# Optimization experiments

Measured on AMD Instinct MI355X. Metric: run time of the kernel, lower is better.

Reference implementation:

```python
import jax, jax.numpy as jnp
import numpy as np

LATENT = 1024
HIDDEN = 1024
VOCAB = 32000
SEQ = 129      # y_len
STRIDE = 128   # number of decode steps = y_len - 1


def setup_inputs() -> dict:
    key = jax.random.key(0)
    ks = jax.random.split(key, 16)
    s = 0.05  # weight scale to keep gates in a sane range
    H, L, V = HIDDEN, LATENT, VOCAB
    return {
        "y": jax.random.randint(ks[0], (SEQ,), 0, V),
        "context_vector": jax.random.normal(ks[1], (2, L), jnp.float32),
        "stride": STRIDE,
        # fc_upscale: latent -> hidden
        "W_up": jax.random.normal(ks[2], (H, L), jnp.float32) * s,
        "b_up": jax.random.normal(ks[3], (H,), jnp.float32) * s,
        # LSTM layer 0 (input_size = 1), torch gate order [i, f, g, o]
        "W_ih0": jax.random.normal(ks[4], (4 * H, 1), jnp.float32) * s,
        "W_hh0": jax.random.normal(ks[5], (4 * H, H), jnp.float32) * s,
        "b_ih0": jax.random.normal(ks[6], (4 * H,), jnp.float32) * s,
        "b_hh0": jax.random.normal(ks[7], (4 * H,), jnp.float32) * s,
        # LSTM layer 1 (input_size = hidden)
        "W_ih1": jax.random.normal(ks[8], (4 * H, H), jnp.float32) * s,
        "W_hh1": jax.random.normal(ks[9], (4 * H, H), jnp.float32) * s,
        "b_ih1": jax.random.normal(ks[10], (4 * H,), jnp.float32) * s,
        "b_hh1": jax.random.normal(ks[11], (4 * H,), jnp.float32) * s,
        # fc_out: hidden -> vocab
        "W_out": jax.random.normal(ks[12], (V, H), jnp.float32) * s,
        "b_out": jax.random.normal(ks[13], (V,), jnp.float32) * s,
    }


def _lstm_cell(x, h, c, Wi, Wh, bi, bh):
    # torch nn.LSTM gate layout: [input, forget, cell(g), output]
    g = Wi @ x + bi + Wh @ h + bh          # [4H]
    i, f, gg, o = jnp.split(g, 4)
    i = jax.nn.sigmoid(i)
    f = jax.nn.sigmoid(f)
    gg = jnp.tanh(gg)
    o = jax.nn.sigmoid(o)
    c2 = f * c + i * gg
    return o * jnp.tanh(c2), c2


def reference(y, context_vector, stride, W_up, b_up,
              W_ih0, W_hh0, b_ih0, b_hh0,
              W_ih1, W_hh1, b_ih1, b_hh1,
              W_out, b_out):
    # non-bidirectional path: ctx = ctx[0] * ctx[1]; both layers share the
    # same upscaled context for h0 and c0 (torch.cat([ctx]*num_layers)).
    ctx = context_vector[0] * context_vector[1]       # [latent]
    h_init = W_up @ ctx + b_up                        # [hidden]
    tok0 = y[0].astype(jnp.float32)

    def step(carry, _):
        h0, c0, h1, c1, tok = carry
        x = tok[None]                                  # [1] LSTM input (token id as float)
        h0, c0 = _lstm_cell(x, h0, c0, W_ih0, W_hh0, b_ih0, b_hh0)
        h1, c1 = _lstm_cell(h0, h1, c1, W_ih1, W_hh1, b_ih1, b_hh1)
        preds = jax.nn.relu(W_out @ h1 + b_out)        # [vocab]
        nxt = jax.lax.stop_gradient(jnp.argmax(preds)).astype(jnp.float32)
        return (h0, c0, h1, c1, nxt), preds

    init = (h_init, h_init, h_init, h_init, tok0)
    _, outputs = jax.lax.scan(step, init, None, length=int(stride))  # [stride, vocab]
    # eval mode: log_softmax over vocab
    return jax.nn.log_softmax(outputs, axis=1)
```

## Files before the change

### kernel.cpp

```cpp
#include <hip/hip_runtime.h>

#define H 1024
#define V 32000
#define NSTEP 128
#define NLOGIT_BLK 8000

#define WS_H0   0
#define WS_C0   2048
#define WS_H1   3072
#define WS_C1   5120
#define WS_TOK  6144
#define WS_LOGZ 6145
#define WS_PMAX 8192
#define WS_PSUM 16384
#define WS_PIDX 24576

__device__ __forceinline__ float wave_dot(const float4* __restrict__ wrow4,
                                          const float4* __restrict__ v4) {
    int lane = threadIdx.x & 63;
    float acc = 0.f;
#pragma unroll
    for (int k = 0; k < 4; ++k) {
        float4 w = wrow4[lane + 64 * k];
        float4 x = v4[lane + 64 * k];
        acc += w.x * x.x + w.y * x.y + w.z * x.z + w.w * x.w;
    }
#pragma unroll
    for (int off = 32; off > 0; off >>= 1)
        acc += __shfl_down(acc, off, 64);
    return acc;
}

__device__ __forceinline__ float sigmoidf_(float x) {
    return 1.f / (1.f + expf(-x));
}

__global__ __launch_bounds__(256) void k_setup(const float* __restrict__ Wup,
                                               const float* __restrict__ bup,
                                               const float* __restrict__ cv,
                                               const int* __restrict__ y,
                                               float* __restrict__ ws) {
    int r = blockIdx.x;
    int t = threadIdx.x;
    __shared__ float red[256];
    const float* row = Wup + (size_t)r * H;
    float acc = 0.f;
    for (int j = t; j < H; j += 256) acc += row[j] * (cv[j] * cv[H + j]);
    red[t] = acc;
    __syncthreads();
    for (int s = 128; s > 0; s >>= 1) {
        if (t < s) red[t] += red[t + s];
        __syncthreads();
    }
    if (t == 0) {
        float h = red[0] + bup[r];
        ws[WS_H0 + r] = h;
        ws[WS_C0 + r] = h;
        ws[WS_H1 + r] = h;
        ws[WS_C1 + r] = h;
        if (r == 0) ws[WS_TOK] = (float)y[0];
    }
}

__global__ __launch_bounds__(256) void k_lstm0(const float* __restrict__ Whh,
                                               const float* __restrict__ Wih_col,
                                               const float* __restrict__ bih,
                                               const float* __restrict__ bhh,
                                               float* __restrict__ ws, int par) {
    __shared__ float4 shv[256];
    __shared__ float gates[4];
    int i = blockIdx.x;
    int t = threadIdx.x;
    const float* hin = ws + WS_H0 + par * H;
    shv[t] = ((const float4*)hin)[t];
    __syncthreads();
    int w = t >> 6;
    int r = i + (w << 10);
    float d = wave_dot((const float4*)(Whh + (size_t)r * H), shv);
    if ((t & 63) == 0) {
        float tok = ws[WS_TOK];
        gates[w] = d + Wih_col[r] * tok + bih[r] + bhh[r];
    }
    __syncthreads();
    if (t == 0) {
        float ig = sigmoidf_(gates[0]);
        float fg = sigmoidf_(gates[1]);
        float gg = tanhf(gates[2]);
        float og = sigmoidf_(gates[3]);
        float c = fg * ws[WS_C0 + i] + ig * gg;
        ws[WS_C0 + i] = c;
        ws[WS_H0 + (par ^ 1) * H + i] = og * tanhf(c);
    }
}

__global__ __launch_bounds__(256) void k_lstm1(const float* __restrict__ Wih,
                                               const float* __restrict__ Whh,
                                               const float* __restrict__ bih,
                                               const float* __restrict__ bhh,
                                               float* __restrict__ ws, int par) {
    __shared__ float4 shx[256];
    __shared__ float4 shh[256];
    __shared__ float gates[4];
    int i = blockIdx.x;
    int t = threadIdx.x;
    shx[t] = ((const float4*)(ws + WS_H0 + (par ^ 1) * H))[t];
    shh[t] = ((const float4*)(ws + WS_H1 + par * H))[t];
    __syncthreads();
    int w = t >> 6;
    int r = i + (w << 10);
    float d = wave_dot((const float4*)(Wih + (size_t)r * H), shx) +
              wave_dot((const float4*)(Whh + (size_t)r * H), shh);
    if ((t & 63) == 0) gates[w] = d + bih[r] + bhh[r];
    __syncthreads();
    if (t == 0) {
        float ig = sigmoidf_(gates[0]);
        float fg = sigmoidf_(gates[1]);
        float gg = tanhf(gates[2]);
        float og = sigmoidf_(gates[3]);
        float c = fg * ws[WS_C1 + i] + ig * gg;
        ws[WS_C1 + i] = c;
        ws[WS_H1 + (par ^ 1) * H + i] = og * tanhf(c);
    }
}

__global__ __launch_bounds__(256) void k_logits(const float* __restrict__ Wout,
                                                const float* __restrict__ bout,
                                                float* __restrict__ outrow,
                                                float* __restrict__ ws, int par) {
    __shared__ float4 shv[256];
    __shared__ float sval[4];
    int b = blockIdx.x;
    int t = threadIdx.x;
    shv[t] = ((const float4*)(ws + WS_H1 + (par ^ 1) * H))[t];
    __syncthreads();
    int w = t >> 6;
    int r = b * 4 + w;
    float d = wave_dot((const float4*)(Wout + (size_t)r * H), shv);
    if ((t & 63) == 0) {
        float v = d + bout[r];
        v = v > 0.f ? v : 0.f;
        outrow[r] = v;
        sval[w] = v;
    }
    __syncthreads();
    if (t == 0) {
        float m = sval[0];
        int mi = 0;
#pragma unroll
        for (int k = 1; k < 4; ++k)
            if (sval[k] > m) { m = sval[k]; mi = k; }
        float s = 0.f;
#pragma unroll
        for (int k = 0; k < 4; ++k) s += expf(sval[k] - m);
        ws[WS_PMAX + b] = m;
        ws[WS_PSUM + b] = s;
        ((int*)ws)[WS_PIDX + b] = b * 4 + mi;
    }
}

__global__ __launch_bounds__(1024) void k_reduce(float* __restrict__ ws) {
    __shared__ float sm[1024];
    __shared__ float ssum[1024];
    __shared__ int si[1024];
    int t = threadIdx.x;
    float m = -1e30f, s = 0.f;
    int idx = 0x7fffffff;
    for (int b = t; b < NLOGIT_BLK; b += 1024) {
        float bm = ws[WS_PMAX + b];
        float bs = ws[WS_PSUM + b];
        int bi = ((int*)ws)[WS_PIDX + b];
        if (bm > m) {
            s = s * expf(m - bm) + bs;
            m = bm;
            idx = bi;
        } else if (bm == m) {
            s += bs;
            if (bi < idx) idx = bi;
        } else {
            s += bs * expf(bm - m);
        }
    }
    sm[t] = m; ssum[t] = s; si[t] = idx;
    __syncthreads();
    for (int o = 512; o > 0; o >>= 1) {
        if (t < o) {
            float m2 = sm[t + o], s2 = ssum[t + o];
            int i2 = si[t + o];
            if (m2 > sm[t]) {
                ssum[t] = ssum[t] * expf(sm[t] - m2) + s2;
                sm[t] = m2;
                si[t] = i2;
            } else if (m2 == sm[t]) {
                ssum[t] += s2;
                if (i2 < si[t]) si[t] = i2;
            } else {
                ssum[t] += s2 * expf(m2 - sm[t]);
            }
        }
        __syncthreads();
    }
    if (t == 0) {
        ws[WS_LOGZ] = sm[0] + logf(ssum[0]);
        ws[WS_TOK] = (float)si[0];
    }
}

__global__ __launch_bounds__(256) void k_norm(float* __restrict__ outrow,
                                              const float* __restrict__ ws) {
    int i = blockIdx.x * 256 + threadIdx.x;
    float lz = ws[WS_LOGZ];
    if (i < V) outrow[i] -= lz;
}

extern "C" void kernel_launch(void* const* d_in, const int* in_sizes, int n_in,
                              void* d_out, int out_size, void* d_ws, size_t ws_size,
                              hipStream_t stream) {
    const int*   y    = (const int*)d_in[0];
    const float* cv   = (const float*)d_in[1];
    const float* Wup  = (const float*)d_in[3];
    const float* bup  = (const float*)d_in[4];
    const float* Wih0 = (const float*)d_in[5];
    const float* Whh0 = (const float*)d_in[6];
    const float* bih0 = (const float*)d_in[7];
    const float* bhh0 = (const float*)d_in[8];
    const float* Wih1 = (const float*)d_in[9];
    const float* Whh1 = (const float*)d_in[10];
    const float* bih1 = (const float*)d_in[11];
    const float* bhh1 = (const float*)d_in[12];
    const float* Wout = (const float*)d_in[13];
    const float* bout = (const float*)d_in[14];
    float* out = (float*)d_out;
    float* ws  = (float*)d_ws;

    k_setup<<<1024, 256, 0, stream>>>(Wup, bup, cv, y, ws);
    for (int t = 0; t < NSTEP; ++t) {
        int par = t & 1;
        k_lstm0<<<1024, 256, 0, stream>>>(Whh0, Wih0, bih0, bhh0, ws, par);
        k_lstm1<<<1024, 256, 0, stream>>>(Wih1, Whh1, bih1, bhh1, ws, par);
        k_logits<<<NLOGIT_BLK, 256, 0, stream>>>(Wout, bout, out + (size_t)t * V, ws, par);
        k_reduce<<<1, 1024, 0, stream>>>(ws);
        k_norm<<<125, 256, 0, stream>>>(out + (size_t)t * V, ws);
    }
}
```

Baseline: 5.730 ms.

## Fuse logits reduction via last-block atomics and batch normalization after loop

The logits kernel now computes 32 rows per block (8 per wave), and the last block to finish, detected by an atomic counter, performs the global max/sum/argmax reduction in-kernel. This removes the separate reduce and per-step normalize launches, so each step needs three kernels instead of five. The log-sum-exp per step is stored and a single grid-stride kernel subtracts it from all rows at the end. The cost is a serialized tail reduction in one block and fewer, larger logits blocks.

```diff
diff --git a/kernel.cpp b/kernel.cpp
--- a/kernel.cpp
+++ b/kernel.cpp
@@ -3,17 +3,20 @@
 #define H 1024
 #define V 32000
 #define NSTEP 128
-#define NLOGIT_BLK 8000
-
-#define WS_H0   0
-#define WS_C0   2048
-#define WS_H1   3072
-#define WS_C1   5120
-#define WS_TOK  6144
-#define WS_LOGZ 6145
-#define WS_PMAX 8192
-#define WS_PSUM 16384
-#define WS_PIDX 24576
+#define LBLK 1000
+#define ROWS_PER_BLK 32
+#define ROWS_PER_WAVE 8
+
+#define WS_H0    0
+#define WS_C0    2048
+#define WS_H1    3072
+#define WS_C1    5120
+#define WS_TOK   6144
+#define WS_LOGZ  6400
+#define WS_PMAX  8192
+#define WS_PSUM  10240
+#define WS_PIDX  12288
+#define WS_CNT   14336
 
 __device__ __forceinline__ float wave_dot(const float4* __restrict__ wrow4,
                                           const float4* __restrict__ v4) {
@@ -52,6 +55,7 @@
         if (t < s) red[t] += red[t + s];
         __syncthreads();
     }
+    if (r == 0 && t < NSTEP) ((int*)ws)[WS_CNT + t] = 0;
     if (t == 0) {
         float h = red[0] + bup[r];
         ws[WS_H0 + r] = h;
@@ -126,90 +130,88 @@
 __global__ __launch_bounds__(256) void k_logits(const float* __restrict__ Wout,
                                                 const float* __restrict__ bout,
                                                 float* __restrict__ outrow,
-                                                float* __restrict__ ws, int par) {
+                                                float* __restrict__ ws,
+                                                int par, int step) {
     __shared__ float4 shv[256];
-    __shared__ float sval[4];
+    __shared__ float wmax[4], wsum[4];
+    __shared__ int widx[4];
+    __shared__ int lastflag;
+    __shared__ float rm[256], rs[256];
+    __shared__ int ri[256];
     int b = blockIdx.x;
     int t = threadIdx.x;
+    int w = t >> 6, lane = t & 63;
     shv[t] = ((const float4*)(ws + WS_H1 + (par ^ 1) * H))[t];
     __syncthreads();
-    int w = t >> 6;
-    int r = b * 4 + w;
-    float d = wave_dot((const float4*)(Wout + (size_t)r * H), shv);
-    if ((t & 63) == 0) {
-        float v = d + bout[r];
-        v = v > 0.f ? v : 0.f;
-        outrow[r] = v;
-        sval[w] = v;
-    }
-    __syncthreads();
-    if (t == 0) {
-        float m = sval[0];
-        int mi = 0;
-#pragma unroll
-        for (int k = 1; k < 4; ++k)
-            if (sval[k] > m) { m = sval[k]; mi = k; }
-        float s = 0.f;
-#pragma unroll
-        for (int k = 0; k < 4; ++k) s += expf(sval[k] - m);
-        ws[WS_PMAX + b] = m;
-        ws[WS_PSUM + b] = s;
-        ((int*)ws)[WS_PIDX + b] = b * 4 + mi;
-    }
-}
-
-__global__ __launch_bounds__(1024) void k_reduce(float* __restrict__ ws) {
-    __shared__ float sm[1024];
-    __shared__ float ssum[1024];
-    __shared__ int si[1024];
-    int t = threadIdx.x;
     float m = -1e30f, s = 0.f;
-    int idx = 0x7fffffff;
-    for (int b = t; b < NLOGIT_BLK; b += 1024) {
-        float bm = ws[WS_PMAX + b];
-        float bs = ws[WS_PSUM + b];
-        int bi = ((int*)ws)[WS_PIDX + b];
-        if (bm > m) {
-            s = s * expf(m - bm) + bs;
-            m = bm;
-            idx = bi;
-        } else if (bm == m) {
-            s += bs;
-            if (bi < idx) idx = bi;
-        } else {
-            s += bs * expf(bm - m);
+    int mi = 0;
+    int rbase = b * ROWS_PER_BLK + w * ROWS_PER_WAVE;
+#pragma unroll
+    for (int k = 0; k < ROWS_PER_WAVE; ++k) {
+        int r = rbase + k;
+        float d = wave_dot((const float4*)(Wout + (size_t)r * H), shv);
+        if (lane == 0) {
+            float v = fmaxf(d + bout[r], 0.f);
+            outrow[r] = v;
+            if (v > m) { s = s * expf(m - v) + 1.f; m = v; mi = r; }
+            else       { s += expf(v - m); }
         }
     }
-    sm[t] = m; ssum[t] = s; si[t] = idx;
-    __syncthreads();
-    for (int o = 512; o > 0; o >>= 1) {
+    if (lane == 0) { wmax[w] = m; wsum[w] = s; widx[w] = mi; }
+    __syncthreads();
+    if (t == 0) {
+        float bm = wmax[0], bs = wsum[0];
+        int bi = widx[0];
+#pragma unroll
+        for (int k = 1; k < 4; ++k) {
+            float m2 = wmax[k], s2 = wsum[k];
+            int i2 = widx[k];
+            if (m2 > bm)      { bs = bs * expf(bm - m2) + s2; bm = m2; bi = i2; }
+            else if (m2 == bm){ bs += s2; if (i2 < bi) bi = i2; }
+            else              { bs += s2 * expf(m2 - bm); }
+        }
+        __hip_atomic_store(ws + WS_PMAX + b, bm, __ATOMIC_RELEASE, __HIP_MEMORY_SCOPE_AGENT);
+        __hip_atomic_store(ws + WS_PSUM + b, bs, __ATOMIC_RELEASE, __HIP_MEMORY_SCOPE_AGENT);
+        __hip_atomic_store((int*)ws + WS_PIDX + b, bi, __ATOMIC_RELEASE, __HIP_MEMORY_SCOPE_AGENT);
+        int old = __hip_atomic_fetch_add((int*)ws + WS_CNT + step, 1,
+                                         __ATOMIC_ACQ_REL, __HIP_MEMORY_SCOPE_AGENT);
+        lastflag = (old == LBLK - 1);
+    }
+    __syncthreads();
+    if (!lastflag) return;
+    float fm = -1e30f, fs = 0.f;
+    int fi = 0x7fffffff;
+    for (int i = t; i < LBLK; i += 256) {
+        float m2 = __hip_atomic_load(ws + WS_PMAX + i, __ATOMIC_ACQUIRE, __HIP_MEMORY_SCOPE_AGENT);
+        float s2 = __hip_atomic_load(ws + WS_PSUM + i, __ATOMIC_ACQUIRE, __HIP_MEMORY_SCOPE_AGENT);
+        int i2 = __hip_atomic_load((int*)ws + WS_PIDX + i, __ATOMIC_ACQUIRE, __HIP_MEMORY_SCOPE_AGENT);
+        if (m2 > fm)       { fs = fs * expf(fm - m2) + s2; fm = m2; fi = i2; }
+        else if (m2 == fm) { fs += s2; if (i2 < fi) fi = i2; }
+        else               { fs += s2 * expf(m2 - fm); }
+    }
+    rm[t] = fm; rs[t] = fs; ri[t] = fi;
+    __syncthreads();
+    for (int o = 128; o > 0; o >>= 1) {
         if (t < o) {
-            float m2 = sm[t + o], s2 = ssum[t + o];
-            int i2 = si[t + o];
-            if (m2 > sm[t]) {
-                ssum[t] = ssum[t] * expf(sm[t] - m2) + s2;
-                sm[t] = m2;
-                si[t] = i2;
-            } else if (m2 == sm[t]) {
-                ssum[t] += s2;
-                if (i2 < si[t]) si[t] = i2;
-            } else {
-                ssum[t] += s2 * expf(m2 - sm[t]);
-            }
+            float m2 = rm[t + o], s2 = rs[t + o];
+            int i2 = ri[t + o];
+            if (m2 > rm[t])       { rs[t] = rs[t] * expf(rm[t] - m2) + s2; rm[t] = m2; ri[t] = i2; }
+            else if (m2 == rm[t]) { rs[t] += s2; if (i2 < ri[t]) ri[t] = i2; }
+            else                  { rs[t] += s2 * expf(m2 - rm[t]); }
         }
         __syncthreads();
     }
     if (t == 0) {
-        ws[WS_LOGZ] = sm[0] + logf(ssum[0]);
-        ws[WS_TOK] = (float)si[0];
-    }
-}
-
-__global__ __launch_bounds__(256) void k_norm(float* __restrict__ outrow,
-                                              const float* __restrict__ ws) {
-    int i = blockIdx.x * 256 + threadIdx.x;
-    float lz = ws[WS_LOGZ];
-    if (i < V) outrow[i] -= lz;
+        ws[WS_LOGZ + step] = rm[0] + logf(rs[0]);
+        ws[WS_TOK] = (float)ri[0];
+    }
+}
+
+__global__ __launch_bounds__(256) void k_norm_all(float* __restrict__ out,
+                                                  const float* __restrict__ ws) {
+    int stride = gridDim.x * 256;
+    for (int i = blockIdx.x * 256 + threadIdx.x; i < NSTEP * V; i += stride)
+        out[i] -= ws[WS_LOGZ + i / V];
 }
 
 extern "C" void kernel_launch(void* const* d_in, const int* in_sizes, int n_in,
@@ -237,8 +239,7 @@
         int par = t & 1;
         k_lstm0<<<1024, 256, 0, stream>>>(Whh0, Wih0, bih0, bhh0, ws, par);
         k_lstm1<<<1024, 256, 0, stream>>>(Wih1, Whh1, bih1, bhh1, ws, par);
-        k_logits<<<NLOGIT_BLK, 256, 0, stream>>>(Wout, bout, out + (size_t)t * V, ws, par);
-        k_reduce<<<1, 1024, 0, stream>>>(ws);
-        k_norm<<<125, 256, 0, stream>>>(out + (size_t)t * V, ws);
-    }
-}
+        k_logits<<<LBLK, 256, 0, stream>>>(Wout, bout, out + (size_t)t * V, ws, par, t);
+    }
+    k_norm_all<<<2048, 256, 0, stream>>>(out, ws);
+}
```

Result: slower. 13.78 ms (+140.6%).

## Fuse decode loop into one persistent cooperative kernel with grid syncs

Applied to the files above, without the earlier changes.

Replaces the 640 per-step kernel launches with a single cooperative persistent kernel of 256 blocks that syncs the grid between the LSTM layers and the logits stage. The argmax/logsumexp reduction is folded into the next step, where every block redundantly reduces the 256 partials, and the log-softmax normalisation is deferred to one pass at the end. This removes launch overhead and per-step global reductions, at the cost of grid-barrier latency and fewer, fatter blocks doing the matvecs. The old multi-kernel path is kept as a fallback if the cooperative launch fails.

```diff
diff --git a/kernel.cpp b/kernel.cpp
--- a/kernel.cpp
+++ b/kernel.cpp
@@ -1,22 +1,255 @@
 #include <hip/hip_runtime.h>
+#include <hip/hip_cooperative_groups.h>
+
+namespace cg = cooperative_groups;
 
 #define H 1024
 #define V 32000
 #define NSTEP 128
-#define NLOGIT_BLK 8000
+#define NBLK 256
+#define NTHR 512
+#define RPB 125
 
 #define WS_H0   0
 #define WS_C0   2048
 #define WS_H1   3072
 #define WS_C1   5120
-#define WS_TOK  6144
-#define WS_LOGZ 6145
-#define WS_PMAX 8192
-#define WS_PSUM 16384
-#define WS_PIDX 24576
-
-__device__ __forceinline__ float wave_dot(const float4* __restrict__ wrow4,
-                                          const float4* __restrict__ v4) {
+#define WS_LOGZ 6144
+#define WS_PM   6400
+#define WS_PS   6656
+#define WS_PI   6912
+
+__device__ __forceinline__ float sigmoidf_(float x) { return 1.f / (1.f + expf(-x)); }
+
+__device__ __forceinline__ float wred(float a) {
+#pragma unroll
+    for (int o = 32; o > 0; o >>= 1) a += __shfl_down(a, o, 64);
+    return a;
+}
+
+__device__ __forceinline__ float dot_row(const float4* __restrict__ w4,
+                                         const float4* h, int lane) {
+    float a = 0.f;
+#pragma unroll
+    for (int k = 0; k < 4; ++k) {
+        float4 w = w4[lane + (k << 6)];
+        a += w.x * h[k].x + w.y * h[k].y + w.z * h[k].z + w.w * h[k].w;
+    }
+    return a;
+}
+
+__global__ __launch_bounds__(NTHR) void k_decoder(
+    const int* __restrict__ y, const float* __restrict__ cv,
+    const float* __restrict__ Wup, const float* __restrict__ bup,
+    const float* __restrict__ Wih0, const float* __restrict__ Whh0,
+    const float* __restrict__ bih0, const float* __restrict__ bhh0,
+    const float* __restrict__ Wih1, const float* __restrict__ Whh1,
+    const float* __restrict__ bih1, const float* __restrict__ bhh1,
+    const float* __restrict__ Wout, const float* __restrict__ bout,
+    float* __restrict__ out, float* __restrict__ ws)
+{
+    cg::grid_group grid = cg::this_grid();
+    const int b = blockIdx.x, t = threadIdx.x;
+    const int w = t >> 6, lane = t & 63;
+    const int gw = (b << 3) + w;
+
+    __shared__ float gl[4][4];
+    __shared__ float pm[8], psv[8];
+    __shared__ int   pix[8];
+    __shared__ float rm[NBLK], rs[NBLK];
+    __shared__ int   ri[NBLK];
+    __shared__ float s_tok;
+
+    if (gw < 1024) {
+        float4 hreg[4];
+#pragma unroll
+        for (int k = 0; k < 4; ++k) {
+            float4 a = ((const float4*)cv)[lane + (k << 6)];
+            float4 c = ((const float4*)(cv + H))[lane + (k << 6)];
+            hreg[k] = make_float4(a.x * c.x, a.y * c.y, a.z * c.z, a.w * c.w);
+        }
+        float acc = wred(dot_row((const float4*)(Wup + (size_t)gw * H), hreg, lane));
+        if (lane == 0) {
+            float h = acc + bup[gw];
+            ws[WS_H0 + gw] = h; ws[WS_C0 + gw] = h;
+            ws[WS_H1 + gw] = h; ws[WS_C1 + gw] = h;
+        }
+    }
+    grid.sync();
+
+    for (int step = 0; step < NSTEP; ++step) {
+        const int p = step & 1;
+
+        float tok;
+        if (step == 0) {
+            tok = (float)y[0];
+        } else {
+            if (t < NBLK) { rm[t] = ws[WS_PM + t]; rs[t] = ws[WS_PS + t]; ri[t] = ((const int*)ws)[WS_PI + t]; }
+            __syncthreads();
+            for (int o = NBLK >> 1; o > 0; o >>= 1) {
+                if (t < o) {
+                    float m2 = rm[t + o], s2 = rs[t + o];
+                    int i2 = ri[t + o];
+                    if (m2 > rm[t])       { rs[t] = rs[t] * expf(rm[t] - m2) + s2; rm[t] = m2; ri[t] = i2; }
+                    else if (m2 == rm[t]) { rs[t] += s2; if (i2 < ri[t]) ri[t] = i2; }
+                    else                  { rs[t] += s2 * expf(m2 - rm[t]); }
+                }
+                __syncthreads();
+            }
+            if (t == 0) {
+                s_tok = (float)ri[0];
+                if (b == 0) ws[WS_LOGZ + step - 1] = rm[0] + logf(rs[0]);
+            }
+            __syncthreads();
+            tok = s_tok;
+        }
+
+        {
+            const float4* h0o = (const float4*)(ws + WS_H0 + p * H);
+            float4 hreg[4];
+#pragma unroll
+            for (int k = 0; k < 4; ++k) hreg[k] = h0o[lane + (k << 6)];
+            const int cell = (b << 2) + (w >> 1);
+            const int r0 = cell + ((w & 1) << 11);
+            const int r1 = r0 + 1024;
+            float a0 = dot_row((const float4*)(Whh0 + (size_t)r0 * H), hreg, lane);
+            float a1 = dot_row((const float4*)(Whh0 + (size_t)r1 * H), hreg, lane);
+            a0 = wred(a0); a1 = wred(a1);
+            if (lane == 0) {
+                int gi = (w & 1) << 1;
+                gl[w >> 1][gi]     = a0 + Wih0[r0] * tok + bih0[r0] + bhh0[r0];
+                gl[w >> 1][gi + 1] = a1 + Wih0[r1] * tok + bih0[r1] + bhh0[r1];
+            }
+            __syncthreads();
+            if (t < 4) {
+                int c = (b << 2) + t;
+                float ig = sigmoidf_(gl[t][0]);
+                float fg = sigmoidf_(gl[t][1]);
+                float gg = tanhf(gl[t][2]);
+                float og = sigmoidf_(gl[t][3]);
+                float cc = fg * ws[WS_C0 + c] + ig * gg;
+                ws[WS_C0 + c] = cc;
+                ws[WS_H0 + (p ^ 1) * H + c] = og * tanhf(cc);
+            }
+        }
+        grid.sync();
+
+        {
+            const float4* h0n = (const float4*)(ws + WS_H0 + (p ^ 1) * H);
+            const float4* h1o = (const float4*)(ws + WS_H1 + p * H);
+            float4 hx[4], hh[4];
+#pragma unroll
+            for (int k = 0; k < 4; ++k) { hx[k] = h0n[lane + (k << 6)]; hh[k] = h1o[lane + (k << 6)]; }
+            const int cell = (b << 2) + (w >> 1);
+            const int r0 = cell + ((w & 1) << 11);
+            const int r1 = r0 + 1024;
+            float a0 = dot_row((const float4*)(Wih1 + (size_t)r0 * H), hx, lane)
+                     + dot_row((const float4*)(Whh1 + (size_t)r0 * H), hh, lane);
+            float a1 = dot_row((const float4*)(Wih1 + (size_t)r1 * H), hx, lane)
+                     + dot_row((const float4*)(Whh1 + (size_t)r1 * H), hh, lane);
+            a0 = wred(a0); a1 = wred(a1);
+            if (lane == 0) {
+                int gi = (w & 1) << 1;
+                gl[w >> 1][gi]     = a0 + bih1[r0] + bhh1[r0];
+                gl[w >> 1][gi + 1] = a1 + bih1[r1] + bhh1[r1];
+            }
+            __syncthreads();
+            if (t < 4) {
+                int c = (b << 2) + t;
+                float ig = sigmoidf_(gl[t][0]);
+                float fg = sigmoidf_(gl[t][1]);
+                float gg = tanhf(gl[t][2]);
+                float og = sigmoidf_(gl[t][3]);
+                float cc = fg * ws[WS_C1 + c] + ig * gg;
+                ws[WS_C1 + c] = cc;
+                ws[WS_H1 + (p ^ 1) * H + c] = og * tanhf(cc);
+            }
+        }
+        grid.sync();
+
+        {
+            const float4* h1n = (const float4*)(ws + WS_H1 + (p ^ 1) * H);
+            float4 hreg[4];
+#pragma unroll
+            for (int k = 0; k < 4; ++k) hreg[k] = h1n[lane + (k << 6)];
+            float* orow = out + (size_t)step * V;
+            const int rbase = b * RPB;
+            int rl = w << 4;
+            const int rend = (w == 7) ? RPB : (rl + 16);
+            float m = -1e30f, s = 0.f;
+            int mi = 0x7fffffff;
+            for (; rl + 1 < rend; rl += 2) {
+                int r = rbase + rl;
+                float a0 = dot_row((const float4*)(Wout + (size_t)r * H), hreg, lane);
+                float a1 = dot_row((const float4*)(Wout + (size_t)(r + 1) * H), hreg, lane);
+                a0 = wred(a0); a1 = wred(a1);
+                if (lane == 0) {
+                    float v0 = fmaxf(a0 + bout[r], 0.f);
+                    float v1 = fmaxf(a1 + bout[r + 1], 0.f);
+                    orow[r] = v0; orow[r + 1] = v1;
+                    if (v0 > m) { s = s * expf(m - v0) + 1.f; m = v0; mi = r; }     else s += expf(v0 - m);
+                    if (v1 > m) { s = s * expf(m - v1) + 1.f; m = v1; mi = r + 1; } else s += expf(v1 - m);
+                }
+            }
+            if (rl < rend) {
+                int r = rbase + rl;
+                float a0 = wred(dot_row((const float4*)(Wout + (size_t)r * H), hreg, lane));
+                if (lane == 0) {
+                    float v0 = fmaxf(a0 + bout[r], 0.f);
+                    orow[r] = v0;
+                    if (v0 > m) { s = s * expf(m - v0) + 1.f; m = v0; mi = r; } else s += expf(v0 - m);
+                }
+            }
+            if (lane == 0) { pm[w] = m; psv[w] = s; pix[w] = mi; }
+            __syncthreads();
+            if (t == 0) {
+                float bm = pm[0], bs = psv[0];
+                int bi = pix[0];
+#pragma unroll
+                for (int k = 1; k < 8; ++k) {
+                    float m2 = pm[k], s2 = psv[k];
+                    int i2 = pix[k];
+                    if (m2 > bm)       { bs = bs * expf(bm - m2) + s2; bm = m2; bi = i2; }
+                    else if (m2 == bm) { bs += s2; if (i2 < bi) bi = i2; }
+                    else               { bs += s2 * expf(m2 - bm); }
+                }
+                ws[WS_PM + b] = bm; ws[WS_PS + b] = bs; ((int*)ws)[WS_PI + b] = bi;
+            }
+        }
+        grid.sync();
+    }
+
+    if (t < NBLK) { rm[t] = ws[WS_PM + t]; rs[t] = ws[WS_PS + t]; }
+    __syncthreads();
+    for (int o = NBLK >> 1; o > 0; o >>= 1) {
+        if (t < o) {
+            float m2 = rm[t + o], s2 = rs[t + o];
+            if (m2 > rm[t])       { rs[t] = rs[t] * expf(rm[t] - m2) + s2; rm[t] = m2; }
+            else if (m2 == rm[t]) { rs[t] += s2; }
+            else                  { rs[t] += s2 * expf(m2 - rm[t]); }
+        }
+        __syncthreads();
+    }
+    if (b == 0 && t == 0) ws[WS_LOGZ + NSTEP - 1] = rm[0] + logf(rs[0]);
+    grid.sync();
+
+    for (int i = b * NTHR + t; i < NSTEP * V; i += NBLK * NTHR)
+        out[i] -= ws[WS_LOGZ + i / V];
+}
+
+#define F_NLB 8000
+#define F_H0    0
+#define F_C0    2048
+#define F_H1    3072
+#define F_C1    5120
+#define F_TOK   6144
+#define F_LOGZ  6145
+#define F_PMAX  8192
+#define F_PSUM  16384
+#define F_PIDX  24576
+
+__device__ __forceinline__ float wave_dot_s(const float4* __restrict__ wrow4,
+                                            const float4* __restrict__ v4) {
     int lane = threadIdx.x & 63;
     float acc = 0.f;
 #pragma unroll
@@ -26,159 +259,118 @@
         acc += w.x * x.x + w.y * x.y + w.z * x.z + w.w * x.w;
     }
 #pragma unroll
-    for (int off = 32; off > 0; off >>= 1)
-        acc += __shfl_down(acc, off, 64);
+    for (int off = 32; off > 0; off >>= 1) acc += __shfl_down(acc, off, 64);
     return acc;
 }
 
-__device__ __forceinline__ float sigmoidf_(float x) {
-    return 1.f / (1.f + expf(-x));
-}
-
-__global__ __launch_bounds__(256) void k_setup(const float* __restrict__ Wup,
+__global__ __launch_bounds__(256) void f_setup(const float* __restrict__ Wup,
                                                const float* __restrict__ bup,
                                                const float* __restrict__ cv,
                                                const int* __restrict__ y,
                                                float* __restrict__ ws) {
-    int r = blockIdx.x;
-    int t = threadIdx.x;
+    int r = blockIdx.x, t = threadIdx.x;
     __shared__ float red[256];
     const float* row = Wup + (size_t)r * H;
     float acc = 0.f;
     for (int j = t; j < H; j += 256) acc += row[j] * (cv[j] * cv[H + j]);
     red[t] = acc;
     __syncthreads();
-    for (int s = 128; s > 0; s >>= 1) {
-        if (t < s) red[t] += red[t + s];
-        __syncthreads();
-    }
+    for (int s = 128; s > 0; s >>= 1) { if (t < s) red[t] += red[t + s]; __syncthreads(); }
     if (t == 0) {
         float h = red[0] + bup[r];
-        ws[WS_H0 + r] = h;
-        ws[WS_C0 + r] = h;
-        ws[WS_H1 + r] = h;
-        ws[WS_C1 + r] = h;
-        if (r == 0) ws[WS_TOK] = (float)y[0];
-    }
-}
-
-__global__ __launch_bounds__(256) void k_lstm0(const float* __restrict__ Whh,
+        ws[F_H0 + r] = h; ws[F_C0 + r] = h; ws[F_H1 + r] = h; ws[F_C1 + r] = h;
+        if (r == 0) ws[F_TOK] = (float)y[0];
+    }
+}
+
+__global__ __launch_bounds__(256) void f_lstm0(const float* __restrict__ Whh,
                                                const float* __restrict__ Wih_col,
                                                const float* __restrict__ bih,
                                                const float* __restrict__ bhh,
                                                float* __restrict__ ws, int par) {
     __shared__ float4 shv[256];
     __shared__ float gates[4];
-    int i = blockIdx.x;
-    int t = threadIdx.x;
-    const float* hin = ws + WS_H0 + par * H;
-    shv[t] = ((const float4*)hin)[t];
-    __syncthreads();
-    int w = t >> 6;
-    int r = i + (w << 10);
-    float d = wave_dot((const float4*)(Whh + (size_t)r * H), shv);
-    if ((t & 63) == 0) {
-        float tok = ws[WS_TOK];
-        gates[w] = d + Wih_col[r] * tok + bih[r] + bhh[r];
-    }
+    int i = blockIdx.x, t = threadIdx.x;
+    shv[t] = ((const float4*)(ws + F_H0 + par * H))[t];
+    __syncthreads();
+    int w = t >> 6, r = i + (w << 10);
+    float d = wave_dot_s((const float4*)(Whh + (size_t)r * H), shv);
+    if ((t & 63) == 0) gates[w] = d + Wih_col[r] * ws[F_TOK] + bih[r] + bhh[r];
     __syncthreads();
     if (t == 0) {
-        float ig = sigmoidf_(gates[0]);
-        float fg = sigmoidf_(gates[1]);
-        float gg = tanhf(gates[2]);
-        float og = sigmoidf_(gates[3]);
-        float c = fg * ws[WS_C0 + i] + ig * gg;
-        ws[WS_C0 + i] = c;
-        ws[WS_H0 + (par ^ 1) * H + i] = og * tanhf(c);
-    }
-}
-
-__global__ __launch_bounds__(256) void k_lstm1(const float* __restrict__ Wih,
+        float ig = sigmoidf_(gates[0]), fg = sigmoidf_(gates[1]);
+        float gg = tanhf(gates[2]), og = sigmoidf_(gates[3]);
+        float c = fg * ws[F_C0 + i] + ig * gg;
+        ws[F_C0 + i] = c;
+        ws[F_H0 + (par ^ 1) * H + i] = og * tanhf(c);
+    }
+}
+
+__global__ __launch_bounds__(256) void f_lstm1(const float* __restrict__ Wih,
                                                const float* __restrict__ Whh,
                                                const float* __restrict__ bih,
                                                const float* __restrict__ bhh,
                                                float* __restrict__ ws, int par) {
-    __shared__ float4 shx[256];
-    __shared__ float4 shh[256];
+    __shared__ float4 shx[256], shh[256];
     __shared__ float gates[4];
-    int i = blockIdx.x;
-    int t = threadIdx.x;
-    shx[t] = ((const float4*)(ws + WS_H0 + (par ^ 1) * H))[t];
-    shh[t] = ((const float4*)(ws + WS_H1 + par * H))[t];
-    __syncthreads();
-    int w = t >> 6;
-    int r = i + (w << 10);
-    float d = wave_dot((const float4*)(Wih + (size_t)r * H), shx) +
-              wave_dot((const float4*)(Whh + (size_t)r * H), shh);
+    int i = blockIdx.x, t = threadIdx.x;
+    shx[t] = ((const float4*)(ws + F_H0 + (par ^ 1) * H))[t];
+    shh[t] = ((const float4*)(ws + F_H1 + par * H))[t];
+    __syncthreads();
+    int w = t >> 6, r = i + (w << 10);
+    float d = wave_dot_s((const float4*)(Wih + (size_t)r * H), shx) +
+              wave_dot_s((const float4*)(Whh + (size_t)r * H), shh);
     if ((t & 63) == 0) gates[w] = d + bih[r] + bhh[r];
     __syncthreads();
     if (t == 0) {
-        float ig = sigmoidf_(gates[0]);
-        float fg = sigmoidf_(gates[1]);
-        float gg = tanhf(gates[2]);
-        float og = sigmoidf_(gates[3]);
-        float c = fg * ws[WS_C1 + i] + ig * gg;
-        ws[WS_C1 + i] = c;
-        ws[WS_H1 + (par ^ 1) * H + i] = og * tanhf(c);
-    }
-}
-
-__global__ __launch_bounds__(256) void k_logits(const float* __restrict__ Wout,
+        float ig = sigmoidf_(gates[0]), fg = sigmoidf_(gates[1]);
+        float gg = tanhf(gates[2]), og = sigmoidf_(gates[3]);
+        float c = fg * ws[F_C1 + i] + ig * gg;
+        ws[F_C1 + i] = c;
+        ws[F_H1 + (par ^ 1) * H + i] = og * tanhf(c);
+    }
+}
+
+__global__ __launch_bounds__(256) void f_logits(const float* __restrict__ Wout,
                                                 const float* __restrict__ bout,
                                                 float* __restrict__ outrow,
                                                 float* __restrict__ ws, int par) {
     __shared__ float4 shv[256];
     __shared__ float sval[4];
-    int b = blockIdx.x;
-    int t = threadIdx.x;
-    shv[t] = ((const float4*)(ws + WS_H1 + (par ^ 1) * H))[t];
-    __syncthreads();
-    int w = t >> 6;
-    int r = b * 4 + w;
-    float d = wave_dot((const float4*)(Wout + (size_t)r * H), shv);
+    int b = blockIdx.x, t = threadIdx.x;
+    shv[t] = ((const float4*)(ws + F_H1 + (par ^ 1) * H))[t];
+    __syncthreads();
+    int w = t >> 6, r = b * 4 + w;
+    float d = wave_dot_s((const float4*)(Wout + (size_t)r * H), shv);
     if ((t & 63) == 0) {
-        float v = d + bout[r];
-        v = v > 0.f ? v : 0.f;
+        float v = fmaxf(d + bout[r], 0.f);
         outrow[r] = v;
         sval[w] = v;
     }
     __syncthreads();
     if (t == 0) {
-        float m = sval[0];
-        int mi = 0;
-#pragma unroll
-        for (int k = 1; k < 4; ++k)
-            if (sval[k] > m) { m = sval[k]; mi = k; }
+        float m = sval[0]; int mi = 0;
+#pragma unroll
+        for (int k = 1; k < 4; ++k) if (sval[k] > m) { m = sval[k]; mi = k; }
         float s = 0.f;
 #pragma unroll
         for (int k = 0; k < 4; ++k) s += expf(sval[k] - m);
-        ws[WS_PMAX + b] = m;
-        ws[WS_PSUM + b] = s;
-        ((int*)ws)[WS_PIDX + b] = b * 4 + mi;
-    }
-}
-
-__global__ __launch_bounds__(1024) void k_reduce(float* __restrict__ ws) {
-    __shared__ float sm[1024];
-    __shared__ float ssum[1024];
+        ws[F_PMAX + b] = m; ws[F_PSUM + b] = s; ((int*)ws)[F_PIDX + b] = b * 4 + mi;
+    }
+}
+
+__global__ __launch_bounds__(1024) void f_reduce(float* __restrict__ ws) {
+    __shared__ float sm[1024], ssum[1024];
     __shared__ int si[1024];
     int t = threadIdx.x;
     float m = -1e30f, s = 0.f;
     int idx = 0x7fffffff;
-    for (int b = t; b < NLOGIT_BLK; b += 1024) {
-        float bm = ws[WS_PMAX + b];
-        float bs = ws[WS_PSUM + b];
-        int bi = ((int*)ws)[WS_PIDX + b];
-        if (bm > m) {
-            s = s * expf(m - bm) + bs;
-            m = bm;
-            idx = bi;
-        } else if (bm == m) {
-            s += bs;
-            if (bi < idx) idx = bi;
-        } else {
-            s += bs * expf(bm - m);
-        }
+    for (int b = t; b < F_NLB; b += 1024) {
+        float bm = ws[F_PMAX + b], bs = ws[F_PSUM + b];
+        int bi = ((int*)ws)[F_PIDX + b];
+        if (bm > m)      { s = s * expf(m - bm) + bs; m = bm; idx = bi; }
+        else if (bm == m){ s += bs; if (bi < idx) idx = bi; }
+        else             { s += bs * expf(bm - m); }
     }
     sm[t] = m; ssum[t] = s; si[t] = idx;
     __syncthreads();
@@ -186,30 +378,19 @@
         if (t < o) {
             float m2 = sm[t + o], s2 = ssum[t + o];
             int i2 = si[t + o];
-            if (m2 > sm[t]) {
-                ssum[t] = ssum[t] * expf(sm[t] - m2) + s2;
-                sm[t] = m2;
-                si[t] = i2;
-            } else if (m2 == sm[t]) {
-                ssum[t] += s2;
-                if (i2 < si[t]) si[t] = i2;
-            } else {
-                ssum[t] += s2 * expf(m2 - sm[t]);
-            }
+            if (m2 > sm[t])       { ssum[t] = ssum[t] * expf(sm[t] - m2) + s2; sm[t] = m2; si[t] = i2; }
+            else if (m2 == sm[t]) { ssum[t] += s2; if (i2 < si[t]) si[t] = i2; }
+            else                  { ssum[t] += s2 * expf(m2 - sm[t]); }
         }
         __syncthreads();
     }
-    if (t == 0) {
-        ws[WS_LOGZ] = sm[0] + logf(ssum[0]);
-        ws[WS_TOK] = (float)si[0];
-    }
-}
-
-__global__ __launch_bounds__(256) void k_norm(float* __restrict__ outrow,
+    if (t == 0) { ws[F_LOGZ] = sm[0] + logf(ssum[0]); ws[F_TOK] = (float)si[0]; }
+}
+
+__global__ __launch_bounds__(256) void f_norm(float* __restrict__ outrow,
                                               const float* __restrict__ ws) {
     int i = blockIdx.x * 256 + threadIdx.x;
-    float lz = ws[WS_LOGZ];
-    if (i < V) outrow[i] -= lz;
+    if (i < V) outrow[i] -= ws[F_LOGZ];
 }
 
 extern "C" void kernel_launch(void* const* d_in, const int* in_sizes, int n_in,
@@ -232,13 +413,23 @@
     float* out = (float*)d_out;
     float* ws  = (float*)d_ws;
 
-    k_setup<<<1024, 256, 0, stream>>>(Wup, bup, cv, y, ws);
-    for (int t = 0; t < NSTEP; ++t) {
-        int par = t & 1;
-        k_lstm0<<<1024, 256, 0, stream>>>(Whh0, Wih0, bih0, bhh0, ws, par);
-        k_lstm1<<<1024, 256, 0, stream>>>(Wih1, Whh1, bih1, bhh1, ws, par);
-        k_logits<<<NLOGIT_BLK, 256, 0, stream>>>(Wout, bout, out + (size_t)t * V, ws, par);
-        k_reduce<<<1, 1024, 0, stream>>>(ws);
-        k_norm<<<125, 256, 0, stream>>>(out + (size_t)t * V, ws);
-    }
-}
+    void* args[] = {
+        (void*)&y, (void*)&cv, (void*)&Wup, (void*)&bup,
+        (void*)&Wih0, (void*)&Whh0, (void*)&bih0, (void*)&bhh0,
+        (void*)&Wih1, (void*)&Whh1, (void*)&bih1, (void*)&bhh1,
+        (void*)&Wout, (void*)&bout, (void*)&out, (void*)&ws
+    };
+    hipError_t err = hipLaunchCooperativeKernel((void*)k_decoder, dim3(NBLK), dim3(NTHR),
+                                                args, 0, stream);
+    if (err != hipSuccess) {
+        f_setup<<<1024, 256, 0, stream>>>(Wup, bup, cv, y, ws);
+        for (int t = 0; t < NSTEP; ++t) {
+            int par = t & 1;
+            f_lstm0<<<1024, 256, 0, stream>>>(Whh0, Wih0, bih0, bhh0, ws, par);
+            f_lstm1<<<1024, 256, 0, stream>>>(Wih1, Whh1, bih1, bhh1, ws, par);
+            f_logits<<<F_NLB, 256, 0, stream>>>(Wout, bout, out + (size_t)t * V, ws, par);
+            f_reduce<<<1, 1024, 0, stream>>>(ws);
+            f_norm<<<125, 256, 0, stream>>>(out + (size_t)t * V, ws);
+        }
+    }
+}
```

New measurement: 13.34 ms. 133% more time.

## Fuse LSTM layers per step, precompute next layer-0 gates, defer log-softmax

Applied to the files above, without the earlier changes.

Merges the two LSTM layer kernels and the argmax reduction into a single per-step kernel. Each block redundantly reduces the previous step's argmax, applies the layer-0 cell elementwise from precomputed gate pre-activations, computes its slice of layer-1 gates, and computes the next step's layer-0 recurrent matvec. The logits kernel now handles 16 rows per block and emits only a partial max and index. Softmax normalisation moves to one batched kernel after all steps. Together these cut per-step launches from five to two, in exchange for redundant argmax and layer-0 elementwise work in every block.

```diff
diff --git a/kernel.cpp b/kernel.cpp
--- a/kernel.cpp
+++ b/kernel.cpp
@@ -3,123 +3,169 @@
 #define H 1024
 #define V 32000
 #define NSTEP 128
-#define NLOGIT_BLK 8000
-
-#define WS_H0   0
-#define WS_C0   2048
-#define WS_H1   3072
-#define WS_C1   5120
-#define WS_TOK  6144
-#define WS_LOGZ 6145
-#define WS_PMAX 8192
-#define WS_PSUM 16384
-#define WS_PIDX 24576
-
-__device__ __forceinline__ float wave_dot(const float4* __restrict__ wrow4,
-                                          const float4* __restrict__ v4) {
-    int lane = threadIdx.x & 63;
-    float acc = 0.f;
+#define LBLK 2000
+#define LROWS 16
+#define NBLK_L 256
+#define NTHR_L 512
+
+#define WS_G0    0
+#define WS_HINIT 8192
+#define WS_C0    9216
+#define WS_H1    11264
+#define WS_C1    13312
+#define WS_PMAX  14336
+#define WS_PIDX  16384
+
+__device__ __forceinline__ float sigmoidf_(float x) { return 1.f / (1.f + expf(-x)); }
+
+__device__ __forceinline__ float wred(float a) {
+#pragma unroll
+    for (int o = 32; o > 0; o >>= 1) a += __shfl_down(a, o, 64);
+    return a;
+}
+
+__device__ __forceinline__ float dot_row(const float4* __restrict__ w4,
+                                         const float4* h, int lane) {
+    float a = 0.f;
 #pragma unroll
     for (int k = 0; k < 4; ++k) {
-        float4 w = wrow4[lane + 64 * k];
-        float4 x = v4[lane + 64 * k];
-        acc += w.x * x.x + w.y * x.y + w.z * x.z + w.w * x.w;
-    }
-#pragma unroll
-    for (int off = 32; off > 0; off >>= 1)
-        acc += __shfl_down(acc, off, 64);
-    return acc;
-}
-
-__device__ __forceinline__ float sigmoidf_(float x) {
-    return 1.f / (1.f + expf(-x));
+        float4 w = w4[lane + (k << 6)];
+        a += w.x * h[k].x + w.y * h[k].y + w.z * h[k].z + w.w * h[k].w;
+    }
+    return a;
 }
 
 __global__ __launch_bounds__(256) void k_setup(const float* __restrict__ Wup,
                                                const float* __restrict__ bup,
                                                const float* __restrict__ cv,
-                                               const int* __restrict__ y,
                                                float* __restrict__ ws) {
-    int r = blockIdx.x;
-    int t = threadIdx.x;
+    int r = blockIdx.x, t = threadIdx.x;
     __shared__ float red[256];
     const float* row = Wup + (size_t)r * H;
     float acc = 0.f;
     for (int j = t; j < H; j += 256) acc += row[j] * (cv[j] * cv[H + j]);
     red[t] = acc;
     __syncthreads();
-    for (int s = 128; s > 0; s >>= 1) {
-        if (t < s) red[t] += red[t + s];
-        __syncthreads();
-    }
+    for (int s = 128; s > 0; s >>= 1) { if (t < s) red[t] += red[t + s]; __syncthreads(); }
     if (t == 0) {
         float h = red[0] + bup[r];
-        ws[WS_H0 + r] = h;
+        ws[WS_HINIT + r] = h;
         ws[WS_C0 + r] = h;
         ws[WS_H1 + r] = h;
         ws[WS_C1 + r] = h;
-        if (r == 0) ws[WS_TOK] = (float)y[0];
-    }
-}
-
-__global__ __launch_bounds__(256) void k_lstm0(const float* __restrict__ Whh,
-                                               const float* __restrict__ Wih_col,
-                                               const float* __restrict__ bih,
-                                               const float* __restrict__ bhh,
-                                               float* __restrict__ ws, int par) {
-    __shared__ float4 shv[256];
-    __shared__ float gates[4];
-    int i = blockIdx.x;
-    int t = threadIdx.x;
-    const float* hin = ws + WS_H0 + par * H;
-    shv[t] = ((const float4*)hin)[t];
-    __syncthreads();
-    int w = t >> 6;
-    int r = i + (w << 10);
-    float d = wave_dot((const float4*)(Whh + (size_t)r * H), shv);
-    if ((t & 63) == 0) {
-        float tok = ws[WS_TOK];
-        gates[w] = d + Wih_col[r] * tok + bih[r] + bhh[r];
-    }
-    __syncthreads();
-    if (t == 0) {
-        float ig = sigmoidf_(gates[0]);
-        float fg = sigmoidf_(gates[1]);
-        float gg = tanhf(gates[2]);
-        float og = sigmoidf_(gates[3]);
-        float c = fg * ws[WS_C0 + i] + ig * gg;
-        ws[WS_C0 + i] = c;
-        ws[WS_H0 + (par ^ 1) * H + i] = og * tanhf(c);
-    }
-}
-
-__global__ __launch_bounds__(256) void k_lstm1(const float* __restrict__ Wih,
-                                               const float* __restrict__ Whh,
-                                               const float* __restrict__ bih,
-                                               const float* __restrict__ bhh,
-                                               float* __restrict__ ws, int par) {
-    __shared__ float4 shx[256];
-    __shared__ float4 shh[256];
-    __shared__ float gates[4];
-    int i = blockIdx.x;
-    int t = threadIdx.x;
-    shx[t] = ((const float4*)(ws + WS_H0 + (par ^ 1) * H))[t];
-    shh[t] = ((const float4*)(ws + WS_H1 + par * H))[t];
-    __syncthreads();
-    int w = t >> 6;
-    int r = i + (w << 10);
-    float d = wave_dot((const float4*)(Wih + (size_t)r * H), shx) +
-              wave_dot((const float4*)(Whh + (size_t)r * H), shh);
-    if ((t & 63) == 0) gates[w] = d + bih[r] + bhh[r];
-    __syncthreads();
-    if (t == 0) {
-        float ig = sigmoidf_(gates[0]);
-        float fg = sigmoidf_(gates[1]);
-        float gg = tanhf(gates[2]);
-        float og = sigmoidf_(gates[3]);
-        float c = fg * ws[WS_C1 + i] + ig * gg;
-        ws[WS_C1 + i] = c;
-        ws[WS_H1 + (par ^ 1) * H + i] = og * tanhf(c);
+    }
+}
+
+__global__ __launch_bounds__(256) void k_g0(const float* __restrict__ Whh0,
+                                            const float* __restrict__ bih0,
+                                            const float* __restrict__ bhh0,
+                                            float* __restrict__ ws) {
+    int b = blockIdx.x, t = threadIdx.x;
+    int w = t >> 6, lane = t & 63;
+    float4 hreg[4];
+#pragma unroll
+    for (int k = 0; k < 4; ++k) hreg[k] = ((const float4*)(ws + WS_HINIT))[lane + (k << 6)];
+    int r = (b << 2) + w;
+    float a = wred(dot_row((const float4*)(Whh0 + (size_t)r * H), hreg, lane));
+    if (lane == 0) ws[WS_G0 + r] = a + bih0[r] + bhh0[r];
+}
+
+__global__ __launch_bounds__(NTHR_L) void k_L(
+    const int* __restrict__ y,
+    const float* __restrict__ Wih0col,
+    const float* __restrict__ Whh0,
+    const float* __restrict__ bih0, const float* __restrict__ bhh0,
+    const float* __restrict__ Wih1, const float* __restrict__ Whh1,
+    const float* __restrict__ bih1, const float* __restrict__ bhh1,
+    float* __restrict__ ws, int step)
+{
+    const int b = blockIdx.x, t = threadIdx.x;
+    const int w = t >> 6, lane = t & 63;
+    const int p = step & 1;
+    __shared__ float h0s[H];
+    __shared__ float rm[NTHR_L];
+    __shared__ int   ri[NTHR_L];
+    __shared__ float gl[4][4];
+
+    float tok;
+    if (step == 0) {
+        tok = (float)y[0];
+    } else {
+        float m = -1e30f;
+        int idx = 0x7fffffff;
+        for (int i = t; i < LBLK; i += NTHR_L) {
+            float m2 = ws[WS_PMAX + i];
+            int i2 = ((const int*)ws)[WS_PIDX + i];
+            if (m2 > m || (m2 == m && i2 < idx)) {
+                if (m2 > m) { m = m2; idx = i2; }
+                else if (i2 < idx) idx = i2;
+            }
+        }
+        rm[t] = m; ri[t] = idx;
+        __syncthreads();
+        for (int o = NTHR_L >> 1; o > 0; o >>= 1) {
+            if (t < o) {
+                float m2 = rm[t + o]; int i2 = ri[t + o];
+                if (m2 > rm[t]) { rm[t] = m2; ri[t] = i2; }
+                else if (m2 == rm[t] && i2 < ri[t]) ri[t] = i2;
+            }
+            __syncthreads();
+        }
+        tok = (float)ri[0];
+    }
+
+    for (int c = t; c < H; c += NTHR_L) {
+        float gi = ws[WS_G0 + p * 4096 + c]        + Wih0col[c]        * tok;
+        float gf = ws[WS_G0 + p * 4096 + 1024 + c] + Wih0col[1024 + c] * tok;
+        float gg = ws[WS_G0 + p * 4096 + 2048 + c] + Wih0col[2048 + c] * tok;
+        float go = ws[WS_G0 + p * 4096 + 3072 + c] + Wih0col[3072 + c] * tok;
+        float cc = sigmoidf_(gf) * ws[WS_C0 + p * H + c] + sigmoidf_(gi) * tanhf(gg);
+        ws[WS_C0 + (p ^ 1) * H + c] = cc;
+        h0s[c] = sigmoidf_(go) * tanhf(cc);
+    }
+    __syncthreads();
+
+    float4 hx[4], hh[4];
+#pragma unroll
+    for (int k = 0; k < 4; ++k) {
+        hx[k] = ((const float4*)h0s)[lane + (k << 6)];
+        hh[k] = ((const float4*)(ws + WS_H1 + p * H))[lane + (k << 6)];
+    }
+    {
+        const int cell = (b << 2) + (w >> 1);
+        const int r0 = cell + ((w & 1) << 11);
+        const int r1 = r0 + 1024;
+        float a0 = dot_row((const float4*)(Wih1 + (size_t)r0 * H), hx, lane)
+                 + dot_row((const float4*)(Whh1 + (size_t)r0 * H), hh, lane);
+        float a1 = dot_row((const float4*)(Wih1 + (size_t)r1 * H), hx, lane)
+                 + dot_row((const float4*)(Whh1 + (size_t)r1 * H), hh, lane);
+        a0 = wred(a0); a1 = wred(a1);
+        if (lane == 0) {
+            int gi = (w & 1) << 1;
+            gl[w >> 1][gi]     = a0 + bih1[r0] + bhh1[r0];
+            gl[w >> 1][gi + 1] = a1 + bih1[r1] + bhh1[r1];
+        }
+    }
+    {
+        const int g0r = (b << 4) + (w << 1);
+        float b0 = dot_row((const float4*)(Whh0 + (size_t)g0r * H), hx, lane);
+        float b1 = dot_row((const float4*)(Whh0 + (size_t)(g0r + 1) * H), hx, lane);
+        b0 = wred(b0); b1 = wred(b1);
+        if (lane == 0) {
+            ws[WS_G0 + (p ^ 1) * 4096 + g0r]     = b0 + bih0[g0r] + bhh0[g0r];
+            ws[WS_G0 + (p ^ 1) * 4096 + g0r + 1] = b1 + bih0[g0r + 1] + bhh0[g0r + 1];
+        }
+    }
+    __syncthreads();
+    if (t < 4) {
+        int cell = (b << 2) + t;
+        float ig = sigmoidf_(gl[t][0]);
+        float fg = sigmoidf_(gl[t][1]);
+        float gg = tanhf(gl[t][2]);
+        float og = sigmoidf_(gl[t][3]);
+        float cc = fg * ws[WS_C1 + cell] + ig * gg;
+        ws[WS_C1 + cell] = cc;
+        ws[WS_H1 + (p ^ 1) * H + cell] = og * tanhf(cc);
     }
 }
 
@@ -127,89 +173,67 @@
                                                 const float* __restrict__ bout,
                                                 float* __restrict__ outrow,
                                                 float* __restrict__ ws, int par) {
-    __shared__ float4 shv[256];
-    __shared__ float sval[4];
-    int b = blockIdx.x;
-    int t = threadIdx.x;
-    shv[t] = ((const float4*)(ws + WS_H1 + (par ^ 1) * H))[t];
-    __syncthreads();
-    int w = t >> 6;
-    int r = b * 4 + w;
-    float d = wave_dot((const float4*)(Wout + (size_t)r * H), shv);
-    if ((t & 63) == 0) {
-        float v = d + bout[r];
-        v = v > 0.f ? v : 0.f;
-        outrow[r] = v;
-        sval[w] = v;
-    }
+    __shared__ float pm[4];
+    __shared__ int   pix[4];
+    int b = blockIdx.x, t = threadIdx.x;
+    int w = t >> 6, lane = t & 63;
+    float4 hreg[4];
+#pragma unroll
+    for (int k = 0; k < 4; ++k)
+        hreg[k] = ((const float4*)(ws + WS_H1 + par * H))[lane + (k << 6)];
+    float m = -1e30f;
+    int mi = 0x7fffffff;
+    const int rbase = b * LROWS + (w << 2);
+#pragma unroll
+    for (int rr = 0; rr < 4; rr += 2) {
+        int r = rbase + rr;
+        float a0 = dot_row((const float4*)(Wout + (size_t)r * H), hreg, lane);
+        float a1 = dot_row((const float4*)(Wout + (size_t)(r + 1) * H), hreg, lane);
+        a0 = wred(a0); a1 = wred(a1);
+        if (lane == 0) {
+            float v0 = fmaxf(a0 + bout[r], 0.f);
+            float v1 = fmaxf(a1 + bout[r + 1], 0.f);
+            outrow[r] = v0; outrow[r + 1] = v1;
+            if (v0 > m) { m = v0; mi = r; }
+            if (v1 > m) { m = v1; mi = r + 1; }
+        }
+    }
+    if (lane == 0) { pm[w] = m; pix[w] = mi; }
     __syncthreads();
     if (t == 0) {
-        float m = sval[0];
-        int mi = 0;
-#pragma unroll
-        for (int k = 1; k < 4; ++k)
-            if (sval[k] > m) { m = sval[k]; mi = k; }
-        float s = 0.f;
-#pragma unroll
-        for (int k = 0; k < 4; ++k) s += expf(sval[k] - m);
-        ws[WS_PMAX + b] = m;
-        ws[WS_PSUM + b] = s;
-        ((int*)ws)[WS_PIDX + b] = b * 4 + mi;
-    }
-}
-
-__global__ __launch_bounds__(1024) void k_reduce(float* __restrict__ ws) {
-    __shared__ float sm[1024];
-    __shared__ float ssum[1024];
-    __shared__ int si[1024];
-    int t = threadIdx.x;
-    float m = -1e30f, s = 0.f;
-    int idx = 0x7fffffff;
-    for (int b = t; b < NLOGIT_BLK; b += 1024) {
-        float bm = ws[WS_PMAX + b];
-        float bs = ws[WS_PSUM + b];
-        int bi = ((int*)ws)[WS_PIDX + b];
-        if (bm > m) {
-            s = s * expf(m - bm) + bs;
-            m = bm;
-            idx = bi;
-        } else if (bm == m) {
-            s += bs;
-            if (bi < idx) idx = bi;
-        } else {
-            s += bs * expf(bm - m);
-        }
-    }
-    sm[t] = m; ssum[t] = s; si[t] = idx;
+        float bm = pm[0]; int bi = pix[0];
+#pragma unroll
+        for (int k = 1; k < 4; ++k) {
+            if (pm[k] > bm) { bm = pm[k]; bi = pix[k]; }
+            else if (pm[k] == bm && pix[k] < bi) bi = pix[k];
+        }
+        ws[WS_PMAX + b] = bm;
+        ((int*)ws)[WS_PIDX + b] = bi;
+    }
+}
+
+__global__ __launch_bounds__(1024) void k_final(float* __restrict__ out) {
+    __shared__ float rm[1024], rs[1024];
+    int s = blockIdx.x, t = threadIdx.x;
+    float* row = out + (size_t)s * V;
+    float m = -1e30f, sum = 0.f;
+    for (int i = t; i < V; i += 1024) {
+        float v = row[i];
+        if (v > m) { sum = sum * expf(m - v) + 1.f; m = v; }
+        else         sum += expf(v - m);
+    }
+    rm[t] = m; rs[t] = sum;
     __syncthreads();
     for (int o = 512; o > 0; o >>= 1) {
         if (t < o) {
-            float m2 = sm[t + o], s2 = ssum[t + o];
-            int i2 = si[t + o];
-            if (m2 > sm[t]) {
-                ssum[t] = ssum[t] * expf(sm[t] - m2) + s2;
-                sm[t] = m2;
-                si[t] = i2;
-            } else if (m2 == sm[t]) {
-                ssum[t] += s2;
-                if (i2 < si[t]) si[t] = i2;
-            } else {
-                ssum[t] += s2 * expf(m2 - sm[t]);
-            }
+            float m2 = rm[t + o], s2 = rs[t + o];
+            if (m2 > rm[t]) { rs[t] = rs[t] * expf(rm[t] - m2) + s2; rm[t] = m2; }
+            else              rs[t] += s2 * expf(m2 - rm[t]);
         }
         __syncthreads();
     }
-    if (t == 0) {
-        ws[WS_LOGZ] = sm[0] + logf(ssum[0]);
-        ws[WS_TOK] = (float)si[0];
-    }
-}
-
-__global__ __launch_bounds__(256) void k_norm(float* __restrict__ outrow,
-                                              const float* __restrict__ ws) {
-    int i = blockIdx.x * 256 + threadIdx.x;
-    float lz = ws[WS_LOGZ];
-    if (i < V) outrow[i] -= lz;
+    float logz = rm[0] + logf(rs[0]);
+    for (int i = t; i < V; i += 1024) row[i] -= logz;
 }
 
 extern "C" void kernel_launch(void* const* d_in, const int* in_sizes, int n_in,
@@ -232,13 +256,12 @@
     float* out = (float*)d_out;
     float* ws  = (float*)d_ws;
 
-    k_setup<<<1024, 256, 0, stream>>>(Wup, bup, cv, y, ws);
+    k_setup<<<1024, 256, 0, stream>>>(Wup, bup, cv, ws);
+    k_g0<<<1024, 256, 0, stream>>>(Whh0, bih0, bhh0, ws);
     for (int t = 0; t < NSTEP; ++t) {
-        int par = t & 1;
-        k_lstm0<<<1024, 256, 0, stream>>>(Whh0, Wih0, bih0, bhh0, ws, par);
-        k_lstm1<<<1024, 256, 0, stream>>>(Wih1, Whh1, bih1, bhh1, ws, par);
-        k_logits<<<NLOGIT_BLK, 256, 0, stream>>>(Wout, bout, out + (size_t)t * V, ws, par);
-        k_reduce<<<1, 1024, 0, stream>>>(ws);
-        k_norm<<<125, 256, 0, stream>>>(out + (size_t)t * V, ws);
-    }
-}
+        k_L<<<NBLK_L, NTHR_L, 0, stream>>>(y, Wih0, Whh0, bih0, bhh0,
+                                           Wih1, Whh1, bih1, bhh1, ws, t);
+        k_logits<<<LBLK, 256, 0, stream>>>(Wout, bout, out + (size_t)t * V, ws, (t & 1) ^ 1);
+    }
+    k_final<<<NSTEP, 1024, 0, stream>>>(out);
+}
```

New measurement: 4.816 ms. 1.19x faster.
